# Kernel optimization log

Measured on AMD Instinct MI355X. Metric: run time of the kernel, lower is better.

The kernel has to match this reference:

```python
import jax, jax.numpy as jnp
import numpy as np

TOP_K = 8
NUM_EXPERTS = 32
CAPACITY = 1024


def setup_inputs() -> dict:
    key = jax.random.key(0)
    k1, k2, k3, k4 = jax.random.split(key, 4)
    B, S, H, E, F = 2, 1024, 1024, NUM_EXPERTS, 768
    return {
        "hidden_states": jax.random.normal(k1, (B, S, H), dtype=jnp.float32),
        "gate_weight": jax.random.normal(k2, (E, H), dtype=jnp.float32) * 0.02,
        "gate_up_proj": jax.random.normal(k3, (E, 2 * F, H), dtype=jnp.float32) * 0.02,
        "down_proj": jax.random.normal(k4, (E, H, F), dtype=jnp.float32) * 0.02,
    }


def reference(hidden_states, gate_weight, gate_up_proj, down_proj):
    B, S, H = hidden_states.shape
    E = gate_weight.shape[0]
    N = B * S
    x = hidden_states.reshape(N, H)

    # Router: fp32 softmax, top-k, renormalize (norm_topk_prob=True)
    logits = x @ gate_weight.T                                   # [N, E]
    probs = jax.nn.softmax(logits.astype(jnp.float32), axis=-1)
    topw, topi = jax.lax.top_k(probs, TOP_K)                     # [N, K]
    topw = topw / topw.sum(-1, keepdims=True)
    topw = topw.astype(x.dtype)

    # Flatten token-slot view (matches repeat_interleave ordering)
    flat_e = topi.reshape(-1)                                    # [N*K] int
    flat_w = topw.reshape(-1)                                    # [N*K]
    flat_x = jnp.repeat(x, TOP_K, axis=0)                        # [N*K, H]

    # Position of each slot within its expert (stable order, like stable argsort)
    oh = jax.nn.one_hot(flat_e, E, dtype=jnp.int32)              # [N*K, E]
    pos = (jnp.cumsum(oh, axis=0) * oh).sum(-1) - 1              # [N*K]

    # Dispatch into per-expert buffers [E, C, H]; grouped GEMMs; gather back
    buf = jnp.zeros((E, CAPACITY, H), x.dtype).at[flat_e, pos].set(flat_x, mode="drop")
    gu = jnp.einsum("ech,efh->ecf", buf, gate_up_proj)           # [E, C, 2F]
    gate, up = jnp.split(gu, 2, axis=-1)
    h = jax.nn.silu(gate) * up                                   # [E, C, F]
    eo = jnp.einsum("ecf,ehf->ech", h, down_proj)                # [E, C, H]
    tok_out = eo.at[flat_e, pos].get(mode="fill", fill_value=0)  # [N*K, H]

    out = (tok_out * flat_w[:, None]).reshape(N, TOP_K, H).sum(1)
    return out.reshape(B, S, H)
```

## Files before the change

### kernel.cpp

```cpp
#include <hip/hip_runtime.h>
#include <stdint.h>
#include <math.h>

#define NTOK  2048
#define HDIM  1024
#define FDIM  768
#define NEXP  32
#define TOPK  8
#define CAP   1024

typedef __attribute__((ext_vector_type(8))) short short8;
typedef __attribute__((ext_vector_type(4))) float f32x4;

__device__ __forceinline__ short f2bf(float f) {
  union { float f; uint32_t u; } c; c.f = f;
  uint32_t u = c.u;
  u += 0x7fffu + ((u >> 16) & 1u);
  return (short)(u >> 16);
}

__device__ __forceinline__ short8 pack8(float4 a, float4 b) {
  short8 r;
  r[0] = f2bf(a.x); r[1] = f2bf(a.y); r[2] = f2bf(a.z); r[3] = f2bf(a.w);
  r[4] = f2bf(b.x); r[5] = f2bf(b.y); r[6] = f2bf(b.z); r[7] = f2bf(b.w);
  return r;
}

__device__ __forceinline__ void gload16(const short* g, short* l) {
  __builtin_amdgcn_global_load_lds(
      (__attribute__((address_space(1))) uint32_t*)g,
      (__attribute__((address_space(3))) uint32_t*)l, 16, 0, 0);
}

__global__ __launch_bounds__(256) void cvt_gup_kern(
    const float* __restrict__ gup, short* __restrict__ W, int f_off) {
  const size_t N8 = (size_t)NEXP * 768 * HDIM / 8;
  const size_t stride = (size_t)gridDim.x * 256;
  for (size_t i = (size_t)blockIdx.x * 256 + threadIdx.x; i < N8; i += stride) {
    const int row = (int)(i >> 7);
    const int k0  = (int)(i & 127) * 8;
    const int e   = row / 768;
    const int rg  = row - e * 768;
    const int half = rg / 384;
    const int fr   = rg - half * 384;
    const size_t src = ((size_t)(e * 1536 + half * 768 + f_off + fr)) * HDIM + k0;
    const float4 a = *(const float4*)(gup + src);
    const float4 b = *(const float4*)(gup + src + 4);
    *(short8*)(W + i * 8) = pack8(a, b);
  }
}

__global__ __launch_bounds__(256) void cvt_dwn_kern(
    const float* __restrict__ dwn, short* __restrict__ W) {
  const size_t N8 = (size_t)NEXP * HDIM * FDIM / 8;
  const size_t stride = (size_t)gridDim.x * 256;
  for (size_t i = (size_t)blockIdx.x * 256 + threadIdx.x; i < N8; i += stride) {
    const float4 a = *(const float4*)(dwn + i * 8);
    const float4 b = *(const float4*)(dwn + i * 8 + 4);
    *(short8*)(W + i * 8) = pack8(a, b);
  }
}

__global__ __launch_bounds__(256) void router_kern(
    const float* __restrict__ x, const float* __restrict__ gw,
    int* __restrict__ cnt, int* __restrict__ slot_tok,
    float* __restrict__ slot_w, short* __restrict__ xb) {
  const int n0 = blockIdx.x * 8;
  const int t  = threadIdx.x;
  __shared__ float ls[8][32];

  const int e = t >> 3;
  const int j = t & 7;
  float acc[8];
#pragma unroll
  for (int i = 0; i < 8; ++i) acc[i] = 0.f;
  const float* gwe = gw + (size_t)e * HDIM;
  for (int i = 0; i < 128; ++i) {
    const int k = j + 8 * i;
    const float gv = gwe[k];
#pragma unroll
    for (int tok = 0; tok < 8; ++tok)
      acc[tok] += gv * x[(size_t)(n0 + tok) * HDIM + k];
  }
#pragma unroll
  for (int tok = 0; tok < 8; ++tok) {
    float v = acc[tok];
    v += __shfl_xor(v, 1); v += __shfl_xor(v, 2); v += __shfl_xor(v, 4);
    if (j == 0) ls[tok][e] = v;
  }
  __syncthreads();

  if (t < 8) {
    const int n = n0 + t;
    float lv[32];
#pragma unroll
    for (int i = 0; i < 32; ++i) lv[i] = ls[t][i];
    int   idx[TOPK];
    float val[TOPK];
    for (int kk = 0; kk < TOPK; ++kk) {
      float best = -INFINITY; int bi = 0;
      for (int i = 0; i < 32; ++i)
        if (lv[i] > best) { best = lv[i]; bi = i; }
      val[kk] = best; idx[kk] = bi; lv[bi] = -INFINITY;
    }
    const float m = val[0];
    float w[TOPK]; float wsum = 0.f;
    for (int kk = 0; kk < TOPK; ++kk) { w[kk] = __expf(val[kk] - m); wsum += w[kk]; }
    const float inv = 1.f / wsum;
    for (int kk = 0; kk < TOPK; ++kk) {
      const int ee = idx[kk];
      const int pos = atomicAdd(&cnt[ee], 1);
      if (pos < CAP) {
        slot_tok[ee * CAP + pos] = n * TOPK + kk;
        slot_w[ee * CAP + pos]   = w[kk] * inv;
      }
    }
  }

  const size_t base = (size_t)n0 * HDIM;
  for (int i = t; i < 8 * HDIM; i += 256)
    xb[base + i] = f2bf(x[base + i]);
}

__global__ __launch_bounds__(256) void gemm1_kern(
    const short* __restrict__ xb, const short* __restrict__ W,
    const int* __restrict__ cnt, const int* __restrict__ slot_tok,
    short* __restrict__ hbuf, int f_off) {
  const int e = blockIdx.z;
  const int mcnt = min(cnt[e], CAP);
  const int r0 = blockIdx.y * 128;
  if (r0 >= mcnt) return;
  const int f0 = blockIdx.x * 64;

  __shared__ short As[128 * 32];
  __shared__ short Bg[64 * 32];
  __shared__ short Bu[64 * 32];

  const int t = threadIdx.x;
  const int wave = t >> 6, lane = t & 63;

  const int la0 = wave * 128 + lane;
  const int la1 = la0 + 64;
  const int arow0 = la0 >> 2, aseg0 = la0 & 3;
  const int arow1 = la1 >> 2, aseg1 = la1 & 3;
  int tok0 = 0, tok1 = 0;
  if (r0 + arow0 < mcnt) tok0 = slot_tok[e * CAP + r0 + arow0] >> 3;
  if (r0 + arow1 < mcnt) tok1 = slot_tok[e * CAP + r0 + arow1] >> 3;
  const short* aSrc0 = xb + (size_t)tok0 * HDIM + aseg0 * 8;
  const short* aSrc1 = xb + (size_t)tok1 * HDIM + aseg1 * 8;
  short* aDst0 = As + wave * 1024;
  short* aDst1 = As + wave * 1024 + 512;

  const int brow = t >> 2, bseg = t & 3;
  const size_t gRow = (size_t)(e * 768 + f0 + brow);
  const size_t uRow = gRow + 384;
  const short* gSrc = W + gRow * HDIM + bseg * 8;
  const short* uSrc = W + uRow * HDIM + bseg * 8;
  short* gDst = Bg + wave * 512;
  short* uDst = Bu + wave * 512;

  const int wm = (wave & 1) * 64, wf = (wave >> 1) * 32;
  const int lrow = lane & 15, lk = (lane >> 4) * 8;

  f32x4 accg[4][2], accu[4][2];
#pragma unroll
  for (int a = 0; a < 4; ++a)
#pragma unroll
    for (int b = 0; b < 2; ++b) {
      accg[a][b] = (f32x4){0.f, 0.f, 0.f, 0.f};
      accu[a][b] = (f32x4){0.f, 0.f, 0.f, 0.f};
    }

  for (int kb = 0; kb < HDIM; kb += 32) {
    gload16(aSrc0 + kb, aDst0);
    gload16(aSrc1 + kb, aDst1);
    gload16(gSrc + kb, gDst);
    gload16(uSrc + kb, uDst);
    __syncthreads();

    short8 af[4], bg[2], bu[2];
#pragma unroll
    for (int mt = 0; mt < 4; ++mt)
      af[mt] = *(const short8*)&As[(wm + mt * 16 + lrow) * 32 + lk];
#pragma unroll
    for (int nt = 0; nt < 2; ++nt) {
      bg[nt] = *(const short8*)&Bg[(wf + nt * 16 + lrow) * 32 + lk];
      bu[nt] = *(const short8*)&Bu[(wf + nt * 16 + lrow) * 32 + lk];
    }
#pragma unroll
    for (int mt = 0; mt < 4; ++mt)
#pragma unroll
      for (int nt = 0; nt < 2; ++nt) {
        accg[mt][nt] = __builtin_amdgcn_mfma_f32_16x16x32_bf16(af[mt], bg[nt], accg[mt][nt], 0, 0, 0);
        accu[mt][nt] = __builtin_amdgcn_mfma_f32_16x16x32_bf16(af[mt], bu[nt], accu[mt][nt], 0, 0, 0);
      }
    __syncthreads();
  }

#pragma unroll
  for (int mt = 0; mt < 4; ++mt)
#pragma unroll
    for (int rr = 0; rr < 4; ++rr) {
      const int pos = r0 + wm + mt * 16 + (lane >> 4) * 4 + rr;
      if (pos < mcnt) {
#pragma unroll
        for (int nt = 0; nt < 2; ++nt) {
          const float g = accg[mt][nt][rr];
          const float u = accu[mt][nt][rr];
          const float hv = (g / (1.f + __expf(-g))) * u;
          hbuf[((size_t)e * CAP + pos) * FDIM + f_off + f0 + wf + nt * 16 + (lane & 15)] = f2bf(hv);
        }
      }
    }
}

__global__ __launch_bounds__(256) void gemm2_kern(
    const short* __restrict__ hbuf, const short* __restrict__ W,
    const int* __restrict__ cnt, const int* __restrict__ slot_tok,
    const float* __restrict__ slot_w, float* __restrict__ out) {
  const int e = blockIdx.z;
  const int mcnt = min(cnt[e], CAP);
  const int r0 = blockIdx.y * 128;
  if (r0 >= mcnt) return;
  const int n0 = blockIdx.x * 128;

  __shared__ short As[128 * 32];
  __shared__ short Bs[128 * 32];

  const int t = threadIdx.x;
  const int wave = t >> 6, lane = t & 63;

  const int l0 = wave * 128 + lane;
  const int l1 = l0 + 64;
  const int ar0 = l0 >> 2, as0 = l0 & 3;
  const int ar1 = l1 >> 2, as1 = l1 & 3;
  const short* aSrc0 = hbuf + ((size_t)e * CAP + r0 + ar0) * FDIM + as0 * 8;
  const short* aSrc1 = hbuf + ((size_t)e * CAP + r0 + ar1) * FDIM + as1 * 8;
  const short* bSrc0 = W + ((size_t)e * HDIM + n0 + ar0) * FDIM + as0 * 8;
  const short* bSrc1 = W + ((size_t)e * HDIM + n0 + ar1) * FDIM + as1 * 8;
  short* aDst0 = As + wave * 1024;
  short* aDst1 = As + wave * 1024 + 512;
  short* bDst0 = Bs + wave * 1024;
  short* bDst1 = Bs + wave * 1024 + 512;

  const int wm = (wave & 1) * 64, wn = (wave >> 1) * 64;
  const int lrow = lane & 15, lk = (lane >> 4) * 8;

  f32x4 acc[4][4];
#pragma unroll
  for (int a = 0; a < 4; ++a)
#pragma unroll
    for (int b = 0; b < 4; ++b) acc[a][b] = (f32x4){0.f, 0.f, 0.f, 0.f};

  for (int kb = 0; kb < FDIM; kb += 32) {
    gload16(aSrc0 + kb, aDst0);
    gload16(aSrc1 + kb, aDst1);
    gload16(bSrc0 + kb, bDst0);
    gload16(bSrc1 + kb, bDst1);
    __syncthreads();

    short8 af[4], bf[4];
#pragma unroll
    for (int i = 0; i < 4; ++i) {
      af[i] = *(const short8*)&As[(wm + i * 16 + lrow) * 32 + lk];
      bf[i] = *(const short8*)&Bs[(wn + i * 16 + lrow) * 32 + lk];
    }
#pragma unroll
    for (int mt = 0; mt < 4; ++mt)
#pragma unroll
      for (int nt = 0; nt < 4; ++nt)
        acc[mt][nt] = __builtin_amdgcn_mfma_f32_16x16x32_bf16(af[mt], bf[nt], acc[mt][nt], 0, 0, 0);
    __syncthreads();
  }

#pragma unroll
  for (int mt = 0; mt < 4; ++mt)
#pragma unroll
    for (int rr = 0; rr < 4; ++rr) {
      const int pos = r0 + wm + mt * 16 + (lane >> 4) * 4 + rr;
      if (pos < mcnt) {
        const int s = slot_tok[e * CAP + pos];
        const float w = slot_w[e * CAP + pos];
        const int n = s >> 3;
        float* orow = out + (size_t)n * HDIM + n0 + wn + (lane & 15);
#pragma unroll
        for (int nt = 0; nt < 4; ++nt)
          atomicAdd(orow + nt * 16, w * acc[mt][nt][rr]);
      }
    }
}

extern "C" void kernel_launch(void* const* d_in, const int* in_sizes, int n_in,
                              void* d_out, int out_size, void* d_ws, size_t ws_size,
                              hipStream_t stream) {
  const float* x   = (const float*)d_in[0];
  const float* gw  = (const float*)d_in[1];
  const float* gup = (const float*)d_in[2];
  const float* dwn = (const float*)d_in[3];
  float* out = (float*)d_out;

  char* ws = (char*)d_ws;
  int*   cnt      = (int*)(ws + 0);
  int*   slot_tok = (int*)(ws + 1024);
  float* slot_w   = (float*)(ws + 1024 + 131072);
  short* xb       = (short*)(ws + 524288);
  short* hbuf     = (short*)(ws + 4718592);
  short* W        = (short*)(ws + 55050240);

  hipMemsetAsync(cnt, 0, 1024, stream);
  hipMemsetAsync(out, 0, (size_t)NTOK * HDIM * sizeof(float), stream);

  router_kern<<<NTOK / 8, 256, 0, stream>>>(x, gw, cnt, slot_tok, slot_w, xb);

  cvt_gup_kern<<<2048, 256, 0, stream>>>(gup, W, 0);
  gemm1_kern<<<dim3(384 / 64, CAP / 128, NEXP), 256, 0, stream>>>(xb, W, cnt, slot_tok, hbuf, 0);
  cvt_gup_kern<<<2048, 256, 0, stream>>>(gup, W, 384);
  gemm1_kern<<<dim3(384 / 64, CAP / 128, NEXP), 256, 0, stream>>>(xb, W, cnt, slot_tok, hbuf, 384);
  cvt_dwn_kern<<<2048, 256, 0, stream>>>(dwn, W);
  gemm2_kern<<<dim3(HDIM / 128, CAP / 128, NEXP), 256, 0, stream>>>(hbuf, W, cnt, slot_tok, slot_w, out);
}
```

Before: 630.4 us.

## Double-buffer GEMM LDS tiles, convert weights once, replace atomics with slot gather

```diff
diff --git a/kernel.cpp b/kernel.cpp
--- a/kernel.cpp
+++ b/kernel.cpp
@@ -33,31 +33,24 @@
 }
 
 __global__ __launch_bounds__(256) void cvt_gup_kern(
-    const float* __restrict__ gup, short* __restrict__ W, int f_off) {
-  const size_t N8 = (size_t)NEXP * 768 * HDIM / 8;
+    const float* __restrict__ gup, short* __restrict__ gupb) {
+  const size_t N8 = (size_t)NEXP * 2 * FDIM * HDIM / 8;
   const size_t stride = (size_t)gridDim.x * 256;
   for (size_t i = (size_t)blockIdx.x * 256 + threadIdx.x; i < N8; i += stride) {
-    const int row = (int)(i >> 7);
-    const int k0  = (int)(i & 127) * 8;
-    const int e   = row / 768;
-    const int rg  = row - e * 768;
-    const int half = rg / 384;
-    const int fr   = rg - half * 384;
-    const size_t src = ((size_t)(e * 1536 + half * 768 + f_off + fr)) * HDIM + k0;
-    const float4 a = *(const float4*)(gup + src);
-    const float4 b = *(const float4*)(gup + src + 4);
-    *(short8*)(W + i * 8) = pack8(a, b);
+    const float4 a = *(const float4*)(gup + i * 8);
+    const float4 b = *(const float4*)(gup + i * 8 + 4);
+    *(short8*)(gupb + i * 8) = pack8(a, b);
   }
 }
 
 __global__ __launch_bounds__(256) void cvt_dwn_kern(
-    const float* __restrict__ dwn, short* __restrict__ W) {
+    const float* __restrict__ dwn, short* __restrict__ dwnb) {
   const size_t N8 = (size_t)NEXP * HDIM * FDIM / 8;
   const size_t stride = (size_t)gridDim.x * 256;
   for (size_t i = (size_t)blockIdx.x * 256 + threadIdx.x; i < N8; i += stride) {
     const float4 a = *(const float4*)(dwn + i * 8);
     const float4 b = *(const float4*)(dwn + i * 8 + 4);
-    *(short8*)(W + i * 8) = pack8(a, b);
+    *(short8*)(dwnb + i * 8) = pack8(a, b);
   }
 }
 
@@ -123,18 +116,18 @@
 }
 
 __global__ __launch_bounds__(256) void gemm1_kern(
-    const short* __restrict__ xb, const short* __restrict__ W,
+    const short* __restrict__ xb, const short* __restrict__ gupb,
     const int* __restrict__ cnt, const int* __restrict__ slot_tok,
-    short* __restrict__ hbuf, int f_off) {
+    short* __restrict__ hbuf) {
   const int e = blockIdx.z;
   const int mcnt = min(cnt[e], CAP);
   const int r0 = blockIdx.y * 128;
   if (r0 >= mcnt) return;
   const int f0 = blockIdx.x * 64;
 
-  __shared__ short As[128 * 32];
-  __shared__ short Bg[64 * 32];
-  __shared__ short Bu[64 * 32];
+  __shared__ short As[2][128 * 32];
+  __shared__ short Bg[2][64 * 32];
+  __shared__ short Bu[2][64 * 32];
 
   const int t = threadIdx.x;
   const int wave = t >> 6, lane = t & 63;
@@ -148,16 +141,10 @@
   if (r0 + arow1 < mcnt) tok1 = slot_tok[e * CAP + r0 + arow1] >> 3;
   const short* aSrc0 = xb + (size_t)tok0 * HDIM + aseg0 * 8;
   const short* aSrc1 = xb + (size_t)tok1 * HDIM + aseg1 * 8;
-  short* aDst0 = As + wave * 1024;
-  short* aDst1 = As + wave * 1024 + 512;
 
   const int brow = t >> 2, bseg = t & 3;
-  const size_t gRow = (size_t)(e * 768 + f0 + brow);
-  const size_t uRow = gRow + 384;
-  const short* gSrc = W + gRow * HDIM + bseg * 8;
-  const short* uSrc = W + uRow * HDIM + bseg * 8;
-  short* gDst = Bg + wave * 512;
-  short* uDst = Bu + wave * 512;
+  const short* gSrc = gupb + ((size_t)e * 1536 + f0 + brow) * HDIM + bseg * 8;
+  const short* uSrc = gupb + ((size_t)e * 1536 + 768 + f0 + brow) * HDIM + bseg * 8;
 
   const int wm = (wave & 1) * 64, wf = (wave >> 1) * 32;
   const int lrow = lane & 15, lk = (lane >> 4) * 8;
@@ -171,21 +158,22 @@
       accu[a][b] = (f32x4){0.f, 0.f, 0.f, 0.f};
     }
 
-  for (int kb = 0; kb < HDIM; kb += 32) {
-    gload16(aSrc0 + kb, aDst0);
-    gload16(aSrc1 + kb, aDst1);
-    gload16(gSrc + kb, gDst);
-    gload16(uSrc + kb, uDst);
-    __syncthreads();
-
+  auto STAGE = [&](int b, int kb) {
+    gload16(aSrc0 + kb, &As[b][wave * 1024]);
+    gload16(aSrc1 + kb, &As[b][wave * 1024 + 512]);
+    gload16(gSrc + kb,  &Bg[b][wave * 512]);
+    gload16(uSrc + kb,  &Bu[b][wave * 512]);
+  };
+
+  auto COMPUTE = [&](int b) {
     short8 af[4], bg[2], bu[2];
 #pragma unroll
     for (int mt = 0; mt < 4; ++mt)
-      af[mt] = *(const short8*)&As[(wm + mt * 16 + lrow) * 32 + lk];
+      af[mt] = *(const short8*)&As[b][(wm + mt * 16 + lrow) * 32 + lk];
 #pragma unroll
     for (int nt = 0; nt < 2; ++nt) {
-      bg[nt] = *(const short8*)&Bg[(wf + nt * 16 + lrow) * 32 + lk];
-      bu[nt] = *(const short8*)&Bu[(wf + nt * 16 + lrow) * 32 + lk];
+      bg[nt] = *(const short8*)&Bg[b][(wf + nt * 16 + lrow) * 32 + lk];
+      bu[nt] = *(const short8*)&Bu[b][(wf + nt * 16 + lrow) * 32 + lk];
     }
 #pragma unroll
     for (int mt = 0; mt < 4; ++mt)
@@ -194,8 +182,18 @@
         accg[mt][nt] = __builtin_amdgcn_mfma_f32_16x16x32_bf16(af[mt], bg[nt], accg[mt][nt], 0, 0, 0);
         accu[mt][nt] = __builtin_amdgcn_mfma_f32_16x16x32_bf16(af[mt], bu[nt], accu[mt][nt], 0, 0, 0);
       }
+  };
+
+  STAGE(0, 0);
+  __syncthreads();
+  int cur = 0;
+  for (int kb = 32; kb < HDIM; kb += 32) {
+    STAGE(cur ^ 1, kb);
+    COMPUTE(cur);
     __syncthreads();
-  }
+    cur ^= 1;
+  }
+  COMPUTE(cur);
 
 #pragma unroll
   for (int mt = 0; mt < 4; ++mt)
@@ -208,24 +206,24 @@
           const float g = accg[mt][nt][rr];
           const float u = accu[mt][nt][rr];
           const float hv = (g / (1.f + __expf(-g))) * u;
-          hbuf[((size_t)e * CAP + pos) * FDIM + f_off + f0 + wf + nt * 16 + (lane & 15)] = f2bf(hv);
+          hbuf[((size_t)e * CAP + pos) * FDIM + f0 + wf + nt * 16 + (lane & 15)] = f2bf(hv);
         }
       }
     }
 }
 
 __global__ __launch_bounds__(256) void gemm2_kern(
-    const short* __restrict__ hbuf, const short* __restrict__ W,
+    const short* __restrict__ hbuf, const short* __restrict__ dwnb,
     const int* __restrict__ cnt, const int* __restrict__ slot_tok,
-    const float* __restrict__ slot_w, float* __restrict__ out) {
+    const float* __restrict__ slot_w, float* __restrict__ slot_out) {
   const int e = blockIdx.z;
   const int mcnt = min(cnt[e], CAP);
   const int r0 = blockIdx.y * 128;
   if (r0 >= mcnt) return;
   const int n0 = blockIdx.x * 128;
 
-  __shared__ short As[128 * 32];
-  __shared__ short Bs[128 * 32];
+  __shared__ short As[2][128 * 32];
+  __shared__ short Bs[2][128 * 32];
 
   const int t = threadIdx.x;
   const int wave = t >> 6, lane = t & 63;
@@ -236,12 +234,8 @@
   const int ar1 = l1 >> 2, as1 = l1 & 3;
   const short* aSrc0 = hbuf + ((size_t)e * CAP + r0 + ar0) * FDIM + as0 * 8;
   const short* aSrc1 = hbuf + ((size_t)e * CAP + r0 + ar1) * FDIM + as1 * 8;
-  const short* bSrc0 = W + ((size_t)e * HDIM + n0 + ar0) * FDIM + as0 * 8;
-  const short* bSrc1 = W + ((size_t)e * HDIM + n0 + ar1) * FDIM + as1 * 8;
-  short* aDst0 = As + wave * 1024;
-  short* aDst1 = As + wave * 1024 + 512;
-  short* bDst0 = Bs + wave * 1024;
-  short* bDst1 = Bs + wave * 1024 + 512;
+  const short* bSrc0 = dwnb + ((size_t)e * HDIM + n0 + ar0) * FDIM + as0 * 8;
+  const short* bSrc1 = dwnb + ((size_t)e * HDIM + n0 + ar1) * FDIM + as1 * 8;
 
   const int wm = (wave & 1) * 64, wn = (wave >> 1) * 64;
   const int lrow = lane & 15, lk = (lane >> 4) * 8;
@@ -252,26 +246,37 @@
 #pragma unroll
     for (int b = 0; b < 4; ++b) acc[a][b] = (f32x4){0.f, 0.f, 0.f, 0.f};
 
-  for (int kb = 0; kb < FDIM; kb += 32) {
-    gload16(aSrc0 + kb, aDst0);
-    gload16(aSrc1 + kb, aDst1);
-    gload16(bSrc0 + kb, bDst0);
-    gload16(bSrc1 + kb, bDst1);
-    __syncthreads();
-
+  auto STAGE = [&](int b, int kb) {
+    gload16(aSrc0 + kb, &As[b][wave * 1024]);
+    gload16(aSrc1 + kb, &As[b][wave * 1024 + 512]);
+    gload16(bSrc0 + kb, &Bs[b][wave * 1024]);
+    gload16(bSrc1 + kb, &Bs[b][wave * 1024 + 512]);
+  };
+
+  auto COMPUTE = [&](int b) {
     short8 af[4], bf[4];
 #pragma unroll
     for (int i = 0; i < 4; ++i) {
-      af[i] = *(const short8*)&As[(wm + i * 16 + lrow) * 32 + lk];
-      bf[i] = *(const short8*)&Bs[(wn + i * 16 + lrow) * 32 + lk];
+      af[i] = *(const short8*)&As[b][(wm + i * 16 + lrow) * 32 + lk];
+      bf[i] = *(const short8*)&Bs[b][(wn + i * 16 + lrow) * 32 + lk];
     }
 #pragma unroll
     for (int mt = 0; mt < 4; ++mt)
 #pragma unroll
       for (int nt = 0; nt < 4; ++nt)
         acc[mt][nt] = __builtin_amdgcn_mfma_f32_16x16x32_bf16(af[mt], bf[nt], acc[mt][nt], 0, 0, 0);
+  };
+
+  STAGE(0, 0);
+  __syncthreads();
+  int cur = 0;
+  for (int kb = 32; kb < FDIM; kb += 32) {
+    STAGE(cur ^ 1, kb);
+    COMPUTE(cur);
     __syncthreads();
-  }
+    cur ^= 1;
+  }
+  COMPUTE(cur);
 
 #pragma unroll
   for (int mt = 0; mt < 4; ++mt)
@@ -281,13 +286,24 @@
       if (pos < mcnt) {
         const int s = slot_tok[e * CAP + pos];
         const float w = slot_w[e * CAP + pos];
-        const int n = s >> 3;
-        float* orow = out + (size_t)n * HDIM + n0 + wn + (lane & 15);
 #pragma unroll
         for (int nt = 0; nt < 4; ++nt)
-          atomicAdd(orow + nt * 16, w * acc[mt][nt][rr]);
+          slot_out[(size_t)s * HDIM + n0 + wn + nt * 16 + (lane & 15)] = w * acc[mt][nt][rr];
       }
     }
+}
+
+__global__ __launch_bounds__(256) void gather_kern(
+    const float* __restrict__ so, float* __restrict__ out) {
+  const int n = blockIdx.x;
+  const int c = threadIdx.x * 4;
+  float4 a = make_float4(0.f, 0.f, 0.f, 0.f);
+#pragma unroll
+  for (int k = 0; k < TOPK; ++k) {
+    const float4 v = *(const float4*)&so[((size_t)(n * TOPK + k)) * HDIM + c];
+    a.x += v.x; a.y += v.y; a.z += v.z; a.w += v.w;
+  }
+  *(float4*)&out[(size_t)n * HDIM + c] = a;
 }
 
 extern "C" void kernel_launch(void* const* d_in, const int* in_sizes, int n_in,
@@ -305,17 +321,15 @@
   float* slot_w   = (float*)(ws + 1024 + 131072);
   short* xb       = (short*)(ws + 524288);
   short* hbuf     = (short*)(ws + 4718592);
-  short* W        = (short*)(ws + 55050240);
+  short* gupb     = (short*)(ws + 55050240);
+  short* dwnb     = (short*)(ws + 155713536);
+  float* slot_out = (float*)(ws + 206045184);
 
   hipMemsetAsync(cnt, 0, 1024, stream);
-  hipMemsetAsync(out, 0, (size_t)NTOK * HDIM * sizeof(float), stream);
-
   router_kern<<<NTOK / 8, 256, 0, stream>>>(x, gw, cnt, slot_tok, slot_w, xb);
-
-  cvt_gup_kern<<<2048, 256, 0, stream>>>(gup, W, 0);
-  gemm1_kern<<<dim3(384 / 64, CAP / 128, NEXP), 256, 0, stream>>>(xb, W, cnt, slot_tok, hbuf, 0);
-  cvt_gup_kern<<<2048, 256, 0, stream>>>(gup, W, 384);
-  gemm1_kern<<<dim3(384 / 64, CAP / 128, NEXP), 256, 0, stream>>>(xb, W, cnt, slot_tok, hbuf, 384);
-  cvt_dwn_kern<<<2048, 256, 0, stream>>>(dwn, W);
-  gemm2_kern<<<dim3(HDIM / 128, CAP / 128, NEXP), 256, 0, stream>>>(hbuf, W, cnt, slot_tok, slot_w, out);
-}
+  cvt_gup_kern<<<2048, 256, 0, stream>>>(gup, gupb);
+  cvt_dwn_kern<<<2048, 256, 0, stream>>>(dwn, dwnb);
+  gemm1_kern<<<dim3(FDIM / 64, CAP / 128, NEXP), 256, 0, stream>>>(xb, gupb, cnt, slot_tok, hbuf);
+  gemm2_kern<<<dim3(HDIM / 128, CAP / 128, NEXP), 256, 0, stream>>>(hbuf, dwnb, cnt, slot_tok, slot_w, slot_out);
+  gather_kern<<<NTOK, 256, 0, stream>>>(slot_out, out);
+}
```

After: 624.1 us. Within noise of the previous version (-1.0%).
